# Optimization experiments

Hardware: AMD Instinct MI355X
Metric: run time of the kernel (lower is better)

## Reference

```python
import jax, jax.numpy as jnp
import numpy as np

N = 50000
E = 800000
NFEAT, NHID, NCODE, NCLASS = 512, 256, 64, 40


def setup_inputs() -> dict:
    key = jax.random.key(0)
    ks = jax.random.split(key, 16)
    def glorot(k, shape):
        lim = 1.0 / np.sqrt(shape[0])
        return jax.random.uniform(k, shape, jnp.float32, -lim, lim)
    return {
        "x": jax.random.normal(ks[0], (N, NFEAT), jnp.float32),
        "edge_src": jax.random.randint(ks[1], (E,), 0, N, jnp.int32),
        "edge_dst": jax.random.randint(ks[2], (E,), 0, N, jnp.int32),
        "edge_weight": jax.random.uniform(ks[3], (E,), jnp.float32),
        "eps": jax.random.normal(ks[4], (N, NCODE), jnp.float32),
        # gc1: GraphConvolution(nfeat, nhid)
        "W1": glorot(ks[5], (NFEAT, NHID)),
        "b1": glorot(ks[6], (NHID,)),
        # fc11 / fc12: Linear(nhid, ncode)
        "W_mu": glorot(ks[7], (NHID, NCODE)),
        "b_mu": glorot(ks[8], (NCODE,)),
        "W_lv": glorot(ks[9], (NHID, NCODE)),
        "b_lv": glorot(ks[10], (NCODE,)),
        # fc2: Linear(ncode, nhid)
        "W_dec": glorot(ks[11], (NCODE, NHID)),
        "b_dec": glorot(ks[12], (NHID,)),
        # gc2: GraphConvolution(2*nhid, nclass)
        "W2": glorot(ks[13], (2 * NHID, NCLASS)),
        "b2": glorot(ks[14], (NCLASS,)),
    }


def spmm(edge_src, edge_dst, edge_weight, support):
    # spmm(adj, support): gather rows at src, scale by edge weight, scatter-add to dst
    msgs = support[edge_src] * edge_weight[:, None]  # [E, d]
    return jax.ops.segment_sum(msgs, edge_dst, num_segments=N)


def reference(x, edge_src, edge_dst, edge_weight, eps,
              W1, b1, W_mu, b_mu, W_lv, b_lv, W_dec, b_dec, W2, b2):
    # gc1: relu(spmm(adj, x @ W1) + b1)
    h1 = jax.nn.relu(spmm(edge_src, edge_dst, edge_weight, x @ W1) + b1)
    # dropout is identity in inference mode
    mu = h1 @ W_mu + b_mu
    log_var = h1 @ W_lv + b_lv
    # reparametrize: std = exp(log_var) (as in source, no 0.5 factor)
    z = mu + eps * jnp.exp(log_var)
    # decode
    x1 = jax.nn.relu(z @ W_dec + b_dec)
    x1 = jnp.concatenate([x1, h1], axis=1)  # [N, 2*nhid]
    # gc2
    logits = spmm(edge_src, edge_dst, edge_weight, x1 @ W2) + b2
    return jax.nn.log_softmax(logits, axis=1)
```

## Files before the change

kernel.cpp:

```cpp
#include <hip/hip_runtime.h>
#include <math.h>

#define N_NODES 50000
#define N_EDGES 800000
#define NFEAT 512
#define NHID 256
#define NCODE 64
#define NCLASS 40
#define NCLS_PAD 48
#define NB_SCAN 196

typedef __attribute__((ext_vector_type(8))) short short8;
typedef __attribute__((ext_vector_type(8))) unsigned short ushort8;
typedef __attribute__((ext_vector_type(4))) unsigned short ushort4v;
typedef __attribute__((ext_vector_type(4))) float floatx4;

__device__ inline unsigned short f2bf(float f) {
    unsigned u = __builtin_bit_cast(unsigned, f);
    u += 0x7fff + ((u >> 16) & 1);
    return (unsigned short)(u >> 16);
}
__device__ inline float bf2f(unsigned short h) {
    return __builtin_bit_cast(float, (unsigned)h << 16);
}
__device__ inline unsigned pkbf(float lo, float hi) {
    unsigned r;
    asm("v_cvt_pk_bf16_f32 %0, %1, %2" : "=v"(r) : "v"(lo), "v"(hi));
    return r;
}
__device__ inline void gload_lds16(const void* g, void* l) {
    __builtin_amdgcn_global_load_lds(
        (const __attribute__((address_space(1))) unsigned int*)g,
        (__attribute__((address_space(3))) unsigned int*)l, 16, 0, 0);
}

__global__ __launch_bounds__(256) void hist_kernel(const int* __restrict__ dst,
                                                   int* __restrict__ counts) {
    int t = blockIdx.x * 256 + threadIdx.x;
    if (t < N_EDGES) atomicAdd(&counts[dst[t]], 1);
}

__global__ __launch_bounds__(256) void scan_block_sums(const int* __restrict__ counts,
                                                       int* __restrict__ blockSums) {
    __shared__ int red[256];
    int t = threadIdx.x;
    int i = blockIdx.x * 256 + t;
    red[t] = (i < N_NODES) ? counts[i] : 0;
    __syncthreads();
#pragma unroll
    for (int off = 128; off > 0; off >>= 1) {
        if (t < off) red[t] += red[t + off];
        __syncthreads();
    }
    if (t == 0) blockSums[blockIdx.x] = red[0];
}

__global__ __launch_bounds__(256) void scan_block_offsets(const int* __restrict__ blockSums,
                                                          int* __restrict__ blockOffsets,
                                                          int* __restrict__ offsets) {
    __shared__ int s[256];
    int t = threadIdx.x;
    int v = (t < NB_SCAN) ? blockSums[t] : 0;
    s[t] = v;
    __syncthreads();
#pragma unroll
    for (int off = 1; off < 256; off <<= 1) {
        int x = (t >= off) ? s[t - off] : 0;
        __syncthreads();
        s[t] += x;
        __syncthreads();
    }
    if (t < NB_SCAN) blockOffsets[t] = s[t] - v;
    if (t == 255) offsets[N_NODES] = s[255];
}

__global__ __launch_bounds__(256) void scan_final(const int* __restrict__ counts,
                                                  const int* __restrict__ blockOffsets,
                                                  int* __restrict__ offsets) {
    __shared__ int s[256];
    int t = threadIdx.x;
    int i = blockIdx.x * 256 + t;
    int v = (i < N_NODES) ? counts[i] : 0;
    s[t] = v;
    __syncthreads();
#pragma unroll
    for (int off = 1; off < 256; off <<= 1) {
        int x = (t >= off) ? s[t - off] : 0;
        __syncthreads();
        s[t] += x;
        __syncthreads();
    }
    if (i < N_NODES) offsets[i] = blockOffsets[blockIdx.x] + s[t] - v;
}

__global__ __launch_bounds__(256) void scatter_kernel(const int* __restrict__ dst,
                                                      const int* __restrict__ src,
                                                      const float* __restrict__ w,
                                                      const int* __restrict__ offsets,
                                                      int* __restrict__ cursor,
                                                      int2* __restrict__ edges) {
    int t = blockIdx.x * 256 + threadIdx.x;
    if (t < N_EDGES) {
        int d = dst[t];
        int pos = offsets[d] + atomicAdd(&cursor[d], 1);
        edges[pos] = make_int2(src[t], __builtin_bit_cast(int, w[t]));
    }
}

__global__ __launch_bounds__(256) void wprep_kernel(const float* __restrict__ W1,
                                                    const float* __restrict__ W2,
                                                    const float* __restrict__ W_mu,
                                                    const float* __restrict__ W_lv,
                                                    const float* __restrict__ W_dec,
                                                    unsigned short* __restrict__ W1t,
                                                    unsigned short* __restrict__ W2bt,
                                                    unsigned short* __restrict__ W_mulvt,
                                                    unsigned short* __restrict__ W_dect) {
    int idx = blockIdx.x * 256 + threadIdx.x;
    if (idx < NFEAT * NHID) {
        int k = idx >> 8;
        int n = idx & 255;
        W1t[(size_t)n * NFEAT + k] = f2bf(W1[idx]);
    } else if (idx < NFEAT * NHID + NCLS_PAD * NFEAT) {
        int i2 = idx - NFEAT * NHID;
        int n = i2 >> 9;
        int k = i2 & 511;
        W2bt[i2] = (n < NCLASS) ? f2bf(W2[(size_t)k * NCLASS + n]) : (unsigned short)0;
    } else if (idx < NFEAT * NHID + NCLS_PAD * NFEAT + 128 * 256) {
        int i2 = idx - NFEAT * NHID - NCLS_PAD * NFEAT;
        int j = i2 >> 8;
        int k = i2 & 255;
        float v = (j < 64) ? W_mu[(size_t)k * NCODE + j] : W_lv[(size_t)k * NCODE + (j - 64)];
        W_mulvt[i2] = f2bf(v);
    } else if (idx < NFEAT * NHID + NCLS_PAD * NFEAT + 128 * 256 + 256 * 64) {
        int i2 = idx - NFEAT * NHID - NCLS_PAD * NFEAT - 128 * 256;
        int n = i2 >> 6;
        int k = i2 & 63;
        W_dect[i2] = f2bf(W_dec[(size_t)k * NHID + n]);
    }
}

__global__ __launch_bounds__(256) void gemm1_mfma(const float* __restrict__ A,
                                                  const unsigned short* __restrict__ Bt,
                                                  unsigned short* __restrict__ C) {
    __shared__ unsigned short As[128 * 64];
    __shared__ unsigned short Bs[128 * 64];
    int t = threadIdx.x;
    int wave = t >> 6, lane = t & 63;
    int quad = lane >> 4, m16 = lane & 15;
    int wr = wave >> 1, wc = wave & 1;
    int m0 = blockIdx.x * 128;
    int n0 = blockIdx.y * 128;

    int srow = t >> 3;
    int kcs = (t & 7) ^ (srow & 7);
    const float* Ap[4];
#pragma unroll
    for (int r = 0; r < 4; ++r) {
        int ga = m0 + r * 32 + srow;
        if (ga >= N_NODES) ga = N_NODES - 1;
        Ap[r] = A + (size_t)ga * NFEAT + kcs * 8;
    }
    const unsigned short* Bbase = Bt + (size_t)(n0 + srow) * NFEAT + kcs * 8;

    floatx4 acc[4][4];
#pragma unroll
    for (int m = 0; m < 4; ++m)
#pragma unroll
        for (int n = 0; n < 4; ++n) acc[m][n] = (floatx4){0.f, 0.f, 0.f, 0.f};

    float4 a0[4], a1[4];
#pragma unroll
    for (int r = 0; r < 4; ++r) {
        a0[r] = *(const float4*)(Ap[r]);
        a1[r] = *(const float4*)(Ap[r] + 4);
    }

#pragma unroll
    for (int k0 = 0; k0 < NFEAT; k0 += 64) {
        uint4 aw[4];
#pragma unroll
        for (int r = 0; r < 4; ++r) {
            aw[r].x = pkbf(a0[r].x, a0[r].y);
            aw[r].y = pkbf(a0[r].z, a0[r].w);
            aw[r].z = pkbf(a1[r].x, a1[r].y);
            aw[r].w = pkbf(a1[r].z, a1[r].w);
        }
        __syncthreads();
#pragma unroll
        for (int r = 0; r < 4; ++r)
            gload_lds16(Bbase + (size_t)r * 32 * NFEAT + k0, &Bs[(r * 256 + wave * 64) * 8]);
#pragma unroll
        for (int r = 0; r < 4; ++r) *(uint4*)&As[(r * 256 + t) * 8] = aw[r];
        __syncthreads();
        if (k0 + 64 < NFEAT) {
#pragma unroll
            for (int r = 0; r < 4; ++r) {
                a0[r] = *(const float4*)(Ap[r] + k0 + 64);
                a1[r] = *(const float4*)(Ap[r] + k0 + 68);
            }
        }
#pragma unroll
        for (int c = 0; c < 2; ++c) {
            int sw = ((c * 4 + quad) ^ (m16 & 7)) * 8;
            short8 af[4], bfr[4];
#pragma unroll
            for (int m = 0; m < 4; ++m)
                af[m] = *(const short8*)&As[(wr * 64 + m * 16 + m16) * 64 + sw];
#pragma unroll
            for (int n = 0; n < 4; ++n)
                bfr[n] = *(const short8*)&Bs[(wc * 64 + n * 16 + m16) * 64 + sw];
#pragma unroll
            for (int m = 0; m < 4; ++m)
#pragma unroll
                for (int n = 0; n < 4; ++n)
                    acc[m][n] =
                        __builtin_amdgcn_mfma_f32_16x16x32_bf16(af[m], bfr[n], acc[m][n], 0, 0, 0);
        }
    }
#pragma unroll
    for (int m = 0; m < 4; ++m) {
#pragma unroll
        for (int n = 0; n < 4; ++n) {
            int col = n0 + wc * 64 + n * 16 + m16;
#pragma unroll
            for (int r = 0; r < 4; ++r) {
                int row = m0 + wr * 64 + m * 16 + quad * 4 + r;
                if (row < N_NODES) C[(size_t)row * NHID + col] = f2bf(acc[m][n][r]);
            }
        }
    }
}

__global__ __launch_bounds__(256) void spmm1_kernel(const int* __restrict__ offsets,
                                                    const int2* __restrict__ edges,
                                                    const unsigned short* __restrict__ S1b,
                                                    const float* __restrict__ b1,
                                                    unsigned short* __restrict__ x1cat) {
    int n = blockIdx.x * 4 + (threadIdx.x >> 6);
    int lane = threadIdx.x & 63;
    int beg = offsets[n], end = offsets[n + 1];
    float ax = 0.f, ay = 0.f, az = 0.f, aw = 0.f;
    int i = beg;
    for (; i + 8 <= end; i += 8) {
        int2 e[8];
        ushort4v r[8];
#pragma unroll
        for (int u = 0; u < 8; u++) e[u] = edges[i + u];
#pragma unroll
        for (int u = 0; u < 8; u++)
            r[u] = *(const ushort4v*)&S1b[(size_t)e[u].x * NHID + lane * 4];
#pragma unroll
        for (int u = 0; u < 8; u++) {
            float ww = __builtin_bit_cast(float, e[u].y);
            ax += ww * bf2f(r[u][0]);
            ay += ww * bf2f(r[u][1]);
            az += ww * bf2f(r[u][2]);
            aw += ww * bf2f(r[u][3]);
        }
    }
    for (; i < end; i++) {
        int2 e = edges[i];
        float ww = __builtin_bit_cast(float, e.y);
        ushort4v r = *(const ushort4v*)&S1b[(size_t)e.x * NHID + lane * 4];
        ax += ww * bf2f(r[0]); ay += ww * bf2f(r[1]);
        az += ww * bf2f(r[2]); aw += ww * bf2f(r[3]);
    }
    float4 bb = *(const float4*)&b1[lane * 4];
    ushort4v hb;
    hb[0] = f2bf(fmaxf(ax + bb.x, 0.f));
    hb[1] = f2bf(fmaxf(ay + bb.y, 0.f));
    hb[2] = f2bf(fmaxf(az + bb.z, 0.f));
    hb[3] = f2bf(fmaxf(aw + bb.w, 0.f));
    *(ushort4v*)&x1cat[(size_t)n * (2 * NHID) + NHID + lane * 4] = hb;
}

__global__ __launch_bounds__(256) void mlp_mfma(const unsigned short* __restrict__ x1cat_ro,
                                                const float* __restrict__ eps,
                                                const float* __restrict__ b_mu,
                                                const float* __restrict__ b_lv,
                                                const unsigned short* __restrict__ W_mulvt,
                                                const float* __restrict__ b_dec,
                                                const unsigned short* __restrict__ W_dect,
                                                unsigned short* __restrict__ x1cat) {
    __shared__ float smulv[16][132];
    __shared__ unsigned short z_bf[16][72];
    int t = threadIdx.x;
    int wave = t >> 6, lane = t & 63;
    int quad = lane >> 4, m16 = lane & 15;
    int node0 = blockIdx.x * 16;

    {
        floatx4 acc[2];
        acc[0] = (floatx4){0.f, 0.f, 0.f, 0.f};
        acc[1] = (floatx4){0.f, 0.f, 0.f, 0.f};
        const unsigned short* Abase =
            x1cat_ro + (size_t)(node0 + m16) * 512 + 256 + quad * 8;
        const unsigned short* Bb0 = W_mulvt + (size_t)(wave * 32 + m16) * 256 + quad * 8;
        const unsigned short* Bb1 = Bb0 + 16 * 256;
#pragma unroll
        for (int k0 = 0; k0 < 256; k0 += 32) {
            short8 afrag = *(const short8*)(Abase + k0);
            short8 bf0 = *(const short8*)(Bb0 + k0);
            short8 bf1 = *(const short8*)(Bb1 + k0);
            acc[0] = __builtin_amdgcn_mfma_f32_16x16x32_bf16(afrag, bf0, acc[0], 0, 0, 0);
            acc[1] = __builtin_amdgcn_mfma_f32_16x16x32_bf16(afrag, bf1, acc[1], 0, 0, 0);
        }
#pragma unroll
        for (int nt = 0; nt < 2; nt++) {
            int j = wave * 32 + nt * 16 + m16;
            float bias = (j < 64) ? b_mu[j] : b_lv[j - 64];
#pragma unroll
            for (int r = 0; r < 4; r++)
                smulv[quad * 4 + r][j] = acc[nt][r] + bias;
        }
    }
    __syncthreads();
#pragma unroll
    for (int r = 0; r < 4; r++) {
        int idx = t + r * 256;
        int n = idx >> 6, j = idx & 63;
        float z = smulv[n][j] + eps[(size_t)node0 * NCODE + idx] * expf(smulv[n][64 + j]);
        z_bf[n][j] = f2bf(z);
    }
    __syncthreads();
    {
        floatx4 acc[4];
#pragma unroll
        for (int i = 0; i < 4; i++) acc[i] = (floatx4){0.f, 0.f, 0.f, 0.f};
#pragma unroll
        for (int ks = 0; ks < 2; ks++) {
            int k0 = ks * 32;
            short8 afrag = *(const short8*)&z_bf[m16][k0 + quad * 8];
#pragma unroll
            for (int nt = 0; nt < 4; nt++) {
                int col = wave * 64 + nt * 16 + m16;
                short8 bfrag = *(const short8*)(W_dect + (size_t)col * 64 + k0 + quad * 8);
                acc[nt] = __builtin_amdgcn_mfma_f32_16x16x32_bf16(afrag, bfrag, acc[nt], 0, 0, 0);
            }
        }
#pragma unroll
        for (int nt = 0; nt < 4; nt++) {
            int col = wave * 64 + nt * 16 + m16;
            float bias = b_dec[col];
#pragma unroll
            for (int r = 0; r < 4; r++) {
                int node = node0 + quad * 4 + r;
                x1cat[(size_t)node * 512 + col] = f2bf(fmaxf(acc[nt][r] + bias, 0.f));
            }
        }
    }
}

__global__ __launch_bounds__(256) void gemm2_mfma(const unsigned short* __restrict__ Xb,
                                                  const unsigned short* __restrict__ Bt,
                                                  unsigned short* __restrict__ S2b) {
    __shared__ unsigned short Bs[NCLS_PAD][520];
    int t = threadIdx.x;
    int wave = t >> 6, lane = t & 63;
    int quad = lane >> 4, m16 = lane & 15;
    int m0 = blockIdx.x * 64;

#pragma unroll
    for (int r = 0; r < 12; ++r) {
        int cidx = r * 256 + t;
        int row = cidx >> 6, col = (cidx & 63) * 8;
        *(ushort8*)&Bs[row][col] = *(const ushort8*)&Bt[(size_t)row * NFEAT + col];
    }

    int arow = m0 + wave * 16 + m16;
    if (arow >= N_NODES) arow = N_NODES - 1;
    const unsigned short* Abase = Xb + (size_t)arow * NFEAT + quad * 8;

    floatx4 acc[3];
#pragma unroll
    for (int i = 0; i < 3; i++) acc[i] = (floatx4){0.f, 0.f, 0.f, 0.f};
    __syncthreads();

#pragma unroll
    for (int k0 = 0; k0 < NFEAT; k0 += 32) {
        short8 af = *(const short8*)(Abase + k0);
#pragma unroll
        for (int nt = 0; nt < 3; nt++) {
            short8 bfr = *(const short8*)&Bs[nt * 16 + m16][k0 + quad * 8];
            acc[nt] = __builtin_amdgcn_mfma_f32_16x16x32_bf16(af, bfr, acc[nt], 0, 0, 0);
        }
    }
#pragma unroll
    for (int nt = 0; nt < 3; nt++) {
        int col = nt * 16 + m16;
        if (col < NCLASS) {
#pragma unroll
            for (int r = 0; r < 4; r++) {
                int row = m0 + wave * 16 + quad * 4 + r;
                if (row < N_NODES) S2b[(size_t)row * NCLASS + col] = f2bf(acc[nt][r]);
            }
        }
    }
}

__global__ __launch_bounds__(256) void spmm2_softmax_kernel(const int* __restrict__ offsets,
                                                            const int2* __restrict__ edges,
                                                            const unsigned short* __restrict__ S2b,
                                                            const float* __restrict__ b2,
                                                            float* __restrict__ out) {
    int wave = threadIdx.x >> 6;
    int lane = threadIdx.x & 63;
    int n = blockIdx.x * 4 + wave;
    int beg = offsets[n], end = offsets[n + 1];
    float acc = 0.f;
    int i = beg;
    for (; i + 4 <= end; i += 4) {
        int2 e0 = edges[i], e1 = edges[i + 1], e2 = edges[i + 2], e3 = edges[i + 3];
        float w0 = __builtin_bit_cast(float, e0.y);
        float w1 = __builtin_bit_cast(float, e1.y);
        float w2 = __builtin_bit_cast(float, e2.y);
        float w3 = __builtin_bit_cast(float, e3.y);
        if (lane < NCLASS) {
            float v0 = bf2f(S2b[(size_t)e0.x * NCLASS + lane]);
            float v1 = bf2f(S2b[(size_t)e1.x * NCLASS + lane]);
            float v2 = bf2f(S2b[(size_t)e2.x * NCLASS + lane]);
            float v3 = bf2f(S2b[(size_t)e3.x * NCLASS + lane]);
            acc += w0 * v0 + w1 * v1 + w2 * v2 + w3 * v3;
        }
    }
    for (; i < end; i++) {
        int2 e = edges[i];
        float ww = __builtin_bit_cast(float, e.y);
        if (lane < NCLASS) acc += ww * bf2f(S2b[(size_t)e.x * NCLASS + lane]);
    }
    float v = (lane < NCLASS) ? (acc + b2[lane]) : -INFINITY;
    float m = v;
#pragma unroll
    for (int off = 32; off > 0; off >>= 1) m = fmaxf(m, __shfl_xor(m, off));
    float ex = (lane < NCLASS) ? expf(v - m) : 0.f;
    float ssum = ex;
#pragma unroll
    for (int off = 32; off > 0; off >>= 1) ssum += __shfl_xor(ssum, off);
    if (lane < NCLASS) out[(size_t)n * NCLASS + lane] = v - m - logf(ssum);
}

extern "C" void kernel_launch(void* const* d_in, const int* in_sizes, int n_in,
                              void* d_out, int out_size, void* d_ws, size_t ws_size,
                              hipStream_t stream) {
    const float* x     = (const float*)d_in[0];
    const int*   esrc  = (const int*)d_in[1];
    const int*   edst  = (const int*)d_in[2];
    const float* ew    = (const float*)d_in[3];
    const float* eps   = (const float*)d_in[4];
    const float* W1    = (const float*)d_in[5];
    const float* b1    = (const float*)d_in[6];
    const float* W_mu  = (const float*)d_in[7];
    const float* b_mu  = (const float*)d_in[8];
    const float* W_lv  = (const float*)d_in[9];
    const float* b_lv  = (const float*)d_in[10];
    const float* W_dec = (const float*)d_in[11];
    const float* b_dec = (const float*)d_in[12];
    const float* W2    = (const float*)d_in[13];
    const float* b2    = (const float*)d_in[14];
    float* out = (float*)d_out;

    unsigned short* support1b = (unsigned short*)d_ws;
    unsigned short* x1cat = support1b + (size_t)N_NODES * NHID;
    unsigned short* S2b = x1cat + (size_t)N_NODES * 2 * NHID;
    unsigned short* W1t    = S2b + (size_t)N_NODES * NCLASS;
    unsigned short* W2bt   = W1t + (size_t)NHID * NFEAT;
    unsigned short* W_mulvt = W2bt + (size_t)NCLS_PAD * NFEAT;
    unsigned short* W_dect  = W_mulvt + 128 * 256;
    int*   counts   = (int*)(((size_t)(W_dect + 256 * 64) + 3) & ~(size_t)3);
    int*   cursor   = counts + N_NODES;
    int*   offsets  = cursor + N_NODES;
    int*   blockSums    = offsets + N_NODES + 1;
    int*   blockOffsets = blockSums + NB_SCAN;
    int2*  edges    = (int2*)(blockOffsets + NB_SCAN);
    edges = (int2*)(((size_t)edges + 7) & ~(size_t)7);
    size_t need = (size_t)((char*)(edges + N_EDGES) - (char*)d_ws);
    if (ws_size < need) return;

    hipMemsetAsync(counts, 0, 2 * N_NODES * sizeof(int), stream);
    hist_kernel<<<(N_EDGES + 255) / 256, 256, 0, stream>>>(edst, counts);
    scan_block_sums<<<NB_SCAN, 256, 0, stream>>>(counts, blockSums);
    scan_block_offsets<<<1, 256, 0, stream>>>(blockSums, blockOffsets, offsets);
    scan_final<<<NB_SCAN, 256, 0, stream>>>(counts, blockOffsets, offsets);
    scatter_kernel<<<(N_EDGES + 255) / 256, 256, 0, stream>>>(edst, esrc, ew, offsets, cursor,
                                                              edges);

    wprep_kernel<<<800, 256, 0, stream>>>(W1, W2, W_mu, W_lv, W_dec, W1t, W2bt, W_mulvt, W_dect);
    dim3 g1((N_NODES + 127) / 128, 2);
    gemm1_mfma<<<g1, 256, 0, stream>>>(x, W1t, support1b);
    spmm1_kernel<<<N_NODES / 4, 256, 0, stream>>>(offsets, edges, support1b, b1, x1cat);
    mlp_mfma<<<N_NODES / 16, 256, 0, stream>>>(x1cat, eps, b_mu, b_lv, W_mulvt, b_dec, W_dect,
                                               x1cat);
    gemm2_mfma<<<(N_NODES + 63) / 64, 256, 0, stream>>>(x1cat, W2bt, S2b);
    spmm2_softmax_kernel<<<N_NODES / 4, 256, 0, stream>>>(offsets, edges, S2b, b2, out);
}
```

Baseline: 452.2 us.

## Fuse first SpMM aggregation with the VAE MLP kernel via shared-memory h1 tile

Merges spmm1 and mlp_mfma into one kernel. Each block aggregates 16 nodes, one wave per four nodes, and keeps the relu'd h1 rows in a swizzled LDS tile that feeds the mu/logvar MFMA directly, so the MLP no longer re-reads h1 from global memory and one launch is dropped. h1 is still written to x1cat for gemm2. The cost is less memory-level parallelism per block, since each wave now walks four nodes one after another, and extra LDS use that may lower occupancy.

```diff
diff --git a/kernel.cpp b/kernel.cpp
--- a/kernel.cpp
+++ b/kernel.cpp
@@ -232,77 +232,78 @@
     }
 }
 
-__global__ __launch_bounds__(256) void spmm1_kernel(const int* __restrict__ offsets,
-                                                    const int2* __restrict__ edges,
-                                                    const unsigned short* __restrict__ S1b,
-                                                    const float* __restrict__ b1,
-                                                    unsigned short* __restrict__ x1cat) {
-    int n = blockIdx.x * 4 + (threadIdx.x >> 6);
-    int lane = threadIdx.x & 63;
-    int beg = offsets[n], end = offsets[n + 1];
-    float ax = 0.f, ay = 0.f, az = 0.f, aw = 0.f;
-    int i = beg;
-    for (; i + 8 <= end; i += 8) {
-        int2 e[8];
-        ushort4v r[8];
-#pragma unroll
-        for (int u = 0; u < 8; u++) e[u] = edges[i + u];
-#pragma unroll
-        for (int u = 0; u < 8; u++)
-            r[u] = *(const ushort4v*)&S1b[(size_t)e[u].x * NHID + lane * 4];
-#pragma unroll
-        for (int u = 0; u < 8; u++) {
-            float ww = __builtin_bit_cast(float, e[u].y);
-            ax += ww * bf2f(r[u][0]);
-            ay += ww * bf2f(r[u][1]);
-            az += ww * bf2f(r[u][2]);
-            aw += ww * bf2f(r[u][3]);
-        }
-    }
-    for (; i < end; i++) {
-        int2 e = edges[i];
-        float ww = __builtin_bit_cast(float, e.y);
-        ushort4v r = *(const ushort4v*)&S1b[(size_t)e.x * NHID + lane * 4];
-        ax += ww * bf2f(r[0]); ay += ww * bf2f(r[1]);
-        az += ww * bf2f(r[2]); aw += ww * bf2f(r[3]);
-    }
-    float4 bb = *(const float4*)&b1[lane * 4];
-    ushort4v hb;
-    hb[0] = f2bf(fmaxf(ax + bb.x, 0.f));
-    hb[1] = f2bf(fmaxf(ay + bb.y, 0.f));
-    hb[2] = f2bf(fmaxf(az + bb.z, 0.f));
-    hb[3] = f2bf(fmaxf(aw + bb.w, 0.f));
-    *(ushort4v*)&x1cat[(size_t)n * (2 * NHID) + NHID + lane * 4] = hb;
-}
-
-__global__ __launch_bounds__(256) void mlp_mfma(const unsigned short* __restrict__ x1cat_ro,
-                                                const float* __restrict__ eps,
-                                                const float* __restrict__ b_mu,
-                                                const float* __restrict__ b_lv,
-                                                const unsigned short* __restrict__ W_mulvt,
-                                                const float* __restrict__ b_dec,
-                                                const unsigned short* __restrict__ W_dect,
-                                                unsigned short* __restrict__ x1cat) {
+__global__ __launch_bounds__(256) void spmm1_mlp_kernel(
+    const int* __restrict__ offsets, const int2* __restrict__ edges,
+    const unsigned short* __restrict__ S1b, const float* __restrict__ b1,
+    const float* __restrict__ eps, const float* __restrict__ b_mu,
+    const float* __restrict__ b_lv, const unsigned short* __restrict__ W_mulvt,
+    const float* __restrict__ b_dec, const unsigned short* __restrict__ W_dect,
+    unsigned short* __restrict__ x1cat) {
+    __shared__ unsigned short h1s[16 * 256];
     __shared__ float smulv[16][132];
     __shared__ unsigned short z_bf[16][72];
     int t = threadIdx.x;
     int wave = t >> 6, lane = t & 63;
     int quad = lane >> 4, m16 = lane & 15;
     int node0 = blockIdx.x * 16;
+
+    float4 bb = *(const float4*)&b1[lane * 4];
+#pragma unroll
+    for (int s = 0; s < 4; ++s) {
+        int n = wave * 4 + s;
+        int node = node0 + n;
+        int beg = offsets[node], end = offsets[node + 1];
+        float ax = 0.f, ay = 0.f, az = 0.f, aw = 0.f;
+        int i = beg;
+        for (; i + 8 <= end; i += 8) {
+            int2 e[8];
+            ushort4v r[8];
+#pragma unroll
+            for (int u = 0; u < 8; u++) e[u] = edges[i + u];
+#pragma unroll
+            for (int u = 0; u < 8; u++)
+                r[u] = *(const ushort4v*)&S1b[(size_t)e[u].x * NHID + lane * 4];
+#pragma unroll
+            for (int u = 0; u < 8; u++) {
+                float ww = __builtin_bit_cast(float, e[u].y);
+                ax += ww * bf2f(r[u][0]);
+                ay += ww * bf2f(r[u][1]);
+                az += ww * bf2f(r[u][2]);
+                aw += ww * bf2f(r[u][3]);
+            }
+        }
+        for (; i < end; i++) {
+            int2 e = edges[i];
+            float ww = __builtin_bit_cast(float, e.y);
+            ushort4v r = *(const ushort4v*)&S1b[(size_t)e.x * NHID + lane * 4];
+            ax += ww * bf2f(r[0]);
+            ay += ww * bf2f(r[1]);
+            az += ww * bf2f(r[2]);
+            aw += ww * bf2f(r[3]);
+        }
+        ushort4v hb;
+        hb[0] = f2bf(fmaxf(ax + bb.x, 0.f));
+        hb[1] = f2bf(fmaxf(ay + bb.y, 0.f));
+        hb[2] = f2bf(fmaxf(az + bb.z, 0.f));
+        hb[3] = f2bf(fmaxf(aw + bb.w, 0.f));
+        *(ushort4v*)&x1cat[(size_t)node * (2 * NHID) + NHID + lane * 4] = hb;
+        int chunk = (lane >> 1) ^ (n & 7);
+        *(ushort4v*)&h1s[n * 256 + chunk * 8 + (lane & 1) * 4] = hb;
+    }
+    __syncthreads();
 
     {
         floatx4 acc[2];
         acc[0] = (floatx4){0.f, 0.f, 0.f, 0.f};
         acc[1] = (floatx4){0.f, 0.f, 0.f, 0.f};
-        const unsigned short* Abase =
-            x1cat_ro + (size_t)(node0 + m16) * 512 + 256 + quad * 8;
         const unsigned short* Bb0 = W_mulvt + (size_t)(wave * 32 + m16) * 256 + quad * 8;
         const unsigned short* Bb1 = Bb0 + 16 * 256;
 #pragma unroll
-        for (int k0 = 0; k0 < 256; k0 += 32) {
-            short8 afrag = *(const short8*)(Abase + k0);
-            short8 bf0 = *(const short8*)(Bb0 + k0);
-            short8 bf1 = *(const short8*)(Bb1 + k0);
+        for (int j = 0; j < 8; ++j) {
+            int chunk = (quad + 4 * j) ^ (m16 & 7);
+            short8 afrag = *(const short8*)&h1s[m16 * 256 + chunk * 8];
+            short8 bf0 = *(const short8*)(Bb0 + j * 32);
+            short8 bf1 = *(const short8*)(Bb1 + j * 32);
             acc[0] = __builtin_amdgcn_mfma_f32_16x16x32_bf16(afrag, bf0, acc[0], 0, 0, 0);
             acc[1] = __builtin_amdgcn_mfma_f32_16x16x32_bf16(afrag, bf1, acc[1], 0, 0, 0);
         }
@@ -488,9 +489,8 @@
     wprep_kernel<<<800, 256, 0, stream>>>(W1, W2, W_mu, W_lv, W_dec, W1t, W2bt, W_mulvt, W_dect);
     dim3 g1((N_NODES + 127) / 128, 2);
     gemm1_mfma<<<g1, 256, 0, stream>>>(x, W1t, support1b);
-    spmm1_kernel<<<N_NODES / 4, 256, 0, stream>>>(offsets, edges, support1b, b1, x1cat);
-    mlp_mfma<<<N_NODES / 16, 256, 0, stream>>>(x1cat, eps, b_mu, b_lv, W_mulvt, b_dec, W_dect,
-                                               x1cat);
+    spmm1_mlp_kernel<<<N_NODES / 16, 256, 0, stream>>>(offsets, edges, support1b, b1, eps, b_mu,
+                                                       b_lv, W_mulvt, b_dec, W_dect, x1cat);
     gemm2_mfma<<<(N_NODES + 63) / 64, 256, 0, stream>>>(x1cat, W2bt, S2b);
     spmm2_softmax_kernel<<<N_NODES / 4, 256, 0, stream>>>(offsets, edges, S2b, b2, out);
 }
```

After: 447.6 us. Within noise of the previous version (-1.0%).

## Fuse MLP reparametrization, decoder and gc2 GEMM into one per-wave kernel

Applied to the files above, without the earlier changes.

Merges the mlp kernel and the gc2 GEMM into a single kernel where each wave owns 16 nodes and keeps the decoded x1 in LDS, so the concatenated [N,512] intermediate is never written to or re-read from global memory. spmm1 now writes a compact h1 buffer. W_mu/W_lv are interleaved in the prepped weight so each wave computes matching mu and log_var tiles in registers and applies the reparametrization without a block-level shared buffer or syncs. The cost is higher register use (16 accumulator tiles plus 8 for mu/lv), weights read from global/L2 per wave instead of being staged in LDS, and one kernel launch removed.

```diff
diff --git a/kernel.cpp b/kernel.cpp
--- a/kernel.cpp
+++ b/kernel.cpp
@@ -130,7 +130,9 @@
         int i2 = idx - NFEAT * NHID - NCLS_PAD * NFEAT;
         int j = i2 >> 8;
         int k = i2 & 255;
-        float v = (j < 64) ? W_mu[(size_t)k * NCODE + j] : W_lv[(size_t)k * NCODE + (j - 64)];
+        int q = j >> 5, r5 = j & 31;
+        float v = (r5 < 16) ? W_mu[(size_t)k * NCODE + q * 16 + r5]
+                            : W_lv[(size_t)k * NCODE + q * 16 + (r5 - 16)];
         W_mulvt[i2] = f2bf(v);
     } else if (idx < NFEAT * NHID + NCLS_PAD * NFEAT + 128 * 256 + 256 * 64) {
         int i2 = idx - NFEAT * NHID - NCLS_PAD * NFEAT - 128 * 256;
@@ -236,7 +238,7 @@
                                                     const int2* __restrict__ edges,
                                                     const unsigned short* __restrict__ S1b,
                                                     const float* __restrict__ b1,
-                                                    unsigned short* __restrict__ x1cat) {
+                                                    unsigned short* __restrict__ h1) {
     int n = blockIdx.x * 4 + (threadIdx.x >> 6);
     int lane = threadIdx.x & 63;
     int beg = offsets[n], end = offsets[n + 1];
@@ -272,128 +274,106 @@
     hb[1] = f2bf(fmaxf(ay + bb.y, 0.f));
     hb[2] = f2bf(fmaxf(az + bb.z, 0.f));
     hb[3] = f2bf(fmaxf(aw + bb.w, 0.f));
-    *(ushort4v*)&x1cat[(size_t)n * (2 * NHID) + NHID + lane * 4] = hb;
-}
-
-__global__ __launch_bounds__(256) void mlp_mfma(const unsigned short* __restrict__ x1cat_ro,
-                                                const float* __restrict__ eps,
-                                                const float* __restrict__ b_mu,
-                                                const float* __restrict__ b_lv,
-                                                const unsigned short* __restrict__ W_mulvt,
-                                                const float* __restrict__ b_dec,
-                                                const unsigned short* __restrict__ W_dect,
-                                                unsigned short* __restrict__ x1cat) {
-    __shared__ float smulv[16][132];
-    __shared__ unsigned short z_bf[16][72];
+    *(ushort4v*)&h1[(size_t)n * NHID + lane * 4] = hb;
+}
+
+__global__ __launch_bounds__(256) void mlp_gemm2_kernel(
+    const unsigned short* __restrict__ h1, const float* __restrict__ eps,
+    const float* __restrict__ b_mu, const float* __restrict__ b_lv,
+    const unsigned short* __restrict__ W_mulvt, const float* __restrict__ b_dec,
+    const unsigned short* __restrict__ W_dect, const unsigned short* __restrict__ W2bt,
+    unsigned short* __restrict__ S2b) {
+    __shared__ unsigned short x1s[4][16][264];
+    __shared__ unsigned short zbf[4][16][72];
     int t = threadIdx.x;
     int wave = t >> 6, lane = t & 63;
     int quad = lane >> 4, m16 = lane & 15;
-    int node0 = blockIdx.x * 16;
-
-    {
-        floatx4 acc[2];
-        acc[0] = (floatx4){0.f, 0.f, 0.f, 0.f};
-        acc[1] = (floatx4){0.f, 0.f, 0.f, 0.f};
-        const unsigned short* Abase =
-            x1cat_ro + (size_t)(node0 + m16) * 512 + 256 + quad * 8;
-        const unsigned short* Bb0 = W_mulvt + (size_t)(wave * 32 + m16) * 256 + quad * 8;
-        const unsigned short* Bb1 = Bb0 + 16 * 256;
-#pragma unroll
-        for (int k0 = 0; k0 < 256; k0 += 32) {
-            short8 afrag = *(const short8*)(Abase + k0);
-            short8 bf0 = *(const short8*)(Bb0 + k0);
-            short8 bf1 = *(const short8*)(Bb1 + k0);
-            acc[0] = __builtin_amdgcn_mfma_f32_16x16x32_bf16(afrag, bf0, acc[0], 0, 0, 0);
-            acc[1] = __builtin_amdgcn_mfma_f32_16x16x32_bf16(afrag, bf1, acc[1], 0, 0, 0);
-        }
-#pragma unroll
-        for (int nt = 0; nt < 2; nt++) {
-            int j = wave * 32 + nt * 16 + m16;
-            float bias = (j < 64) ? b_mu[j] : b_lv[j - 64];
-#pragma unroll
-            for (int r = 0; r < 4; r++)
-                smulv[quad * 4 + r][j] = acc[nt][r] + bias;
-        }
-    }
-    __syncthreads();
-#pragma unroll
-    for (int r = 0; r < 4; r++) {
-        int idx = t + r * 256;
-        int n = idx >> 6, j = idx & 63;
-        float z = smulv[n][j] + eps[(size_t)node0 * NCODE + idx] * expf(smulv[n][64 + j]);
-        z_bf[n][j] = f2bf(z);
-    }
-    __syncthreads();
-    {
-        floatx4 acc[4];
-#pragma unroll
-        for (int i = 0; i < 4; i++) acc[i] = (floatx4){0.f, 0.f, 0.f, 0.f};
-#pragma unroll
-        for (int ks = 0; ks < 2; ks++) {
-            int k0 = ks * 32;
-            short8 afrag = *(const short8*)&z_bf[m16][k0 + quad * 8];
-#pragma unroll
-            for (int nt = 0; nt < 4; nt++) {
-                int col = wave * 64 + nt * 16 + m16;
-                short8 bfrag = *(const short8*)(W_dect + (size_t)col * 64 + k0 + quad * 8);
-                acc[nt] = __builtin_amdgcn_mfma_f32_16x16x32_bf16(afrag, bfrag, acc[nt], 0, 0, 0);
-            }
-        }
-#pragma unroll
-        for (int nt = 0; nt < 4; nt++) {
-            int col = wave * 64 + nt * 16 + m16;
-            float bias = b_dec[col];
-#pragma unroll
-            for (int r = 0; r < 4; r++) {
-                int node = node0 + quad * 4 + r;
-                x1cat[(size_t)node * 512 + col] = f2bf(fmaxf(acc[nt][r] + bias, 0.f));
-            }
-        }
-    }
-}
-
-__global__ __launch_bounds__(256) void gemm2_mfma(const unsigned short* __restrict__ Xb,
-                                                  const unsigned short* __restrict__ Bt,
-                                                  unsigned short* __restrict__ S2b) {
-    __shared__ unsigned short Bs[NCLS_PAD][520];
-    int t = threadIdx.x;
-    int wave = t >> 6, lane = t & 63;
-    int quad = lane >> 4, m16 = lane & 15;
-    int m0 = blockIdx.x * 64;
-
-#pragma unroll
-    for (int r = 0; r < 12; ++r) {
-        int cidx = r * 256 + t;
-        int row = cidx >> 6, col = (cidx & 63) * 8;
-        *(ushort8*)&Bs[row][col] = *(const ushort8*)&Bt[(size_t)row * NFEAT + col];
-    }
-
-    int arow = m0 + wave * 16 + m16;
+    int row0 = blockIdx.x * 64 + wave * 16;
+
+    int arow = row0 + m16;
     if (arow >= N_NODES) arow = N_NODES - 1;
-    const unsigned short* Abase = Xb + (size_t)arow * NFEAT + quad * 8;
-
-    floatx4 acc[3];
-#pragma unroll
-    for (int i = 0; i < 3; i++) acc[i] = (floatx4){0.f, 0.f, 0.f, 0.f};
-    __syncthreads();
-
-#pragma unroll
-    for (int k0 = 0; k0 < NFEAT; k0 += 32) {
-        short8 af = *(const short8*)(Abase + k0);
-#pragma unroll
-        for (int nt = 0; nt < 3; nt++) {
-            short8 bfr = *(const short8*)&Bs[nt * 16 + m16][k0 + quad * 8];
-            acc[nt] = __builtin_amdgcn_mfma_f32_16x16x32_bf16(af, bfr, acc[nt], 0, 0, 0);
-        }
-    }
-#pragma unroll
-    for (int nt = 0; nt < 3; nt++) {
+    const unsigned short* Ah = h1 + (size_t)arow * NHID + quad * 8;
+
+    floatx4 amu[4], alv[4];
+#pragma unroll
+    for (int q = 0; q < 4; ++q) {
+        amu[q] = (floatx4){0.f, 0.f, 0.f, 0.f};
+        alv[q] = (floatx4){0.f, 0.f, 0.f, 0.f};
+    }
+#pragma unroll
+    for (int k0 = 0; k0 < NHID; k0 += 32) {
+        short8 af = *(const short8*)(Ah + k0);
+#pragma unroll
+        for (int q = 0; q < 4; ++q) {
+            short8 bm = *(const short8*)(W_mulvt + (size_t)(q * 32 + m16) * 256 + k0 + quad * 8);
+            short8 bl =
+                *(const short8*)(W_mulvt + (size_t)(q * 32 + 16 + m16) * 256 + k0 + quad * 8);
+            amu[q] = __builtin_amdgcn_mfma_f32_16x16x32_bf16(af, bm, amu[q], 0, 0, 0);
+            alv[q] = __builtin_amdgcn_mfma_f32_16x16x32_bf16(af, bl, alv[q], 0, 0, 0);
+        }
+    }
+#pragma unroll
+    for (int q = 0; q < 4; ++q) {
+        int col = q * 16 + m16;
+        float bmu = b_mu[col], blv = b_lv[col];
+#pragma unroll
+        for (int r = 0; r < 4; ++r) {
+            int row = row0 + quad * 4 + r;
+            int er = (row < N_NODES) ? row : N_NODES - 1;
+            float mu = amu[q][r] + bmu;
+            float lv = alv[q][r] + blv;
+            float z = mu + eps[(size_t)er * NCODE + col] * expf(lv);
+            zbf[wave][quad * 4 + r][col] = f2bf(z);
+        }
+    }
+    floatx4 c[16];
+#pragma unroll
+    for (int ct = 0; ct < 16; ++ct) c[ct] = (floatx4){0.f, 0.f, 0.f, 0.f};
+#pragma unroll
+    for (int ks = 0; ks < 2; ++ks) {
+        short8 af = *(const short8*)&zbf[wave][m16][ks * 32 + quad * 8];
+#pragma unroll
+        for (int ct = 0; ct < 16; ++ct) {
+            short8 bfr = *(const short8*)(W_dect + (size_t)(ct * 16 + m16) * 64 + ks * 32 + quad * 8);
+            c[ct] = __builtin_amdgcn_mfma_f32_16x16x32_bf16(af, bfr, c[ct], 0, 0, 0);
+        }
+    }
+#pragma unroll
+    for (int ct = 0; ct < 16; ++ct) {
+        float bias = b_dec[ct * 16 + m16];
+#pragma unroll
+        for (int r = 0; r < 4; ++r)
+            x1s[wave][quad * 4 + r][ct * 16 + m16] = f2bf(fmaxf(c[ct][r] + bias, 0.f));
+    }
+    floatx4 d[3];
+#pragma unroll
+    for (int nt = 0; nt < 3; ++nt) d[nt] = (floatx4){0.f, 0.f, 0.f, 0.f};
+#pragma unroll
+    for (int k0 = 0; k0 < 256; k0 += 32) {
+        short8 af = *(const short8*)&x1s[wave][m16][k0 + quad * 8];
+#pragma unroll
+        for (int nt = 0; nt < 3; ++nt) {
+            short8 bfr = *(const short8*)(W2bt + (size_t)(nt * 16 + m16) * NFEAT + k0 + quad * 8);
+            d[nt] = __builtin_amdgcn_mfma_f32_16x16x32_bf16(af, bfr, d[nt], 0, 0, 0);
+        }
+    }
+#pragma unroll
+    for (int k0 = 256; k0 < 512; k0 += 32) {
+        short8 af = *(const short8*)(Ah + (k0 - 256));
+#pragma unroll
+        for (int nt = 0; nt < 3; ++nt) {
+            short8 bfr = *(const short8*)(W2bt + (size_t)(nt * 16 + m16) * NFEAT + k0 + quad * 8);
+            d[nt] = __builtin_amdgcn_mfma_f32_16x16x32_bf16(af, bfr, d[nt], 0, 0, 0);
+        }
+    }
+#pragma unroll
+    for (int nt = 0; nt < 3; ++nt) {
         int col = nt * 16 + m16;
         if (col < NCLASS) {
 #pragma unroll
-            for (int r = 0; r < 4; r++) {
-                int row = m0 + wave * 16 + quad * 4 + r;
-                if (row < N_NODES) S2b[(size_t)row * NCLASS + col] = f2bf(acc[nt][r]);
+            for (int r = 0; r < 4; ++r) {
+                int row = row0 + quad * 4 + r;
+                if (row < N_NODES) S2b[(size_t)row * NCLASS + col] = f2bf(d[nt][r]);
             }
         }
     }
@@ -461,8 +441,8 @@
     float* out = (float*)d_out;
 
     unsigned short* support1b = (unsigned short*)d_ws;
-    unsigned short* x1cat = support1b + (size_t)N_NODES * NHID;
-    unsigned short* S2b = x1cat + (size_t)N_NODES * 2 * NHID;
+    unsigned short* h1 = support1b + (size_t)N_NODES * NHID;
+    unsigned short* S2b = h1 + (size_t)N_NODES * NHID;
     unsigned short* W1t    = S2b + (size_t)N_NODES * NCLASS;
     unsigned short* W2bt   = W1t + (size_t)NHID * NFEAT;
     unsigned short* W_mulvt = W2bt + (size_t)NCLS_PAD * NFEAT;
@@ -488,9 +468,8 @@
     wprep_kernel<<<800, 256, 0, stream>>>(W1, W2, W_mu, W_lv, W_dec, W1t, W2bt, W_mulvt, W_dect);
     dim3 g1((N_NODES + 127) / 128, 2);
     gemm1_mfma<<<g1, 256, 0, stream>>>(x, W1t, support1b);
-    spmm1_kernel<<<N_NODES / 4, 256, 0, stream>>>(offsets, edges, support1b, b1, x1cat);
-    mlp_mfma<<<N_NODES / 16, 256, 0, stream>>>(x1cat, eps, b_mu, b_lv, W_mulvt, b_dec, W_dect,
-                                               x1cat);
-    gemm2_mfma<<<(N_NODES + 63) / 64, 256, 0, stream>>>(x1cat, W2bt, S2b);
+    spmm1_kernel<<<N_NODES / 4, 256, 0, stream>>>(offsets, edges, support1b, b1, h1);
+    mlp_gemm2_kernel<<<(N_NODES + 63) / 64, 256, 0, stream>>>(h1, eps, b_mu, b_lv, W_mulvt,
+                                                              b_dec, W_dect, W2bt, S2b);
     spmm2_softmax_kernel<<<N_NODES / 4, 256, 0, stream>>>(offsets, edges, S2b, b2, out);
 }
```

Result: slower. 474.6 us (+5.0%).

## Split fused MLP kernel into LDS-tiled mu/logvar GEMM and z-decode GEMM

Applied to the files above, without the earlier changes.

Replaces the fused mlp_mfma kernel, which handled 16 nodes per block and read weights straight from global memory, with two kernels. mulv_mfma tiles 64 nodes per block with the weight slice staged in LDS and writes mu/log_var to a bf16 workspace. zdec_mfma computes z from that buffer and eps in registers, then multiplies by a W_dec held in LDS. The goal is better weight reuse and larger tiles, at the cost of an extra launch, a round trip of the mu/log_var intermediate through global memory, and bf16 rounding of log_var before exp.

```diff
diff --git a/kernel.cpp b/kernel.cpp
--- a/kernel.cpp
+++ b/kernel.cpp
@@ -275,79 +275,112 @@
     *(ushort4v*)&x1cat[(size_t)n * (2 * NHID) + NHID + lane * 4] = hb;
 }
 
-__global__ __launch_bounds__(256) void mlp_mfma(const unsigned short* __restrict__ x1cat_ro,
-                                                const float* __restrict__ eps,
-                                                const float* __restrict__ b_mu,
-                                                const float* __restrict__ b_lv,
-                                                const unsigned short* __restrict__ W_mulvt,
-                                                const float* __restrict__ b_dec,
-                                                const unsigned short* __restrict__ W_dect,
-                                                unsigned short* __restrict__ x1cat) {
-    __shared__ float smulv[16][132];
-    __shared__ unsigned short z_bf[16][72];
+__global__ __launch_bounds__(256) void mulv_mfma(const unsigned short* __restrict__ x1cat,
+                                                 const unsigned short* __restrict__ W_mulvt,
+                                                 const float* __restrict__ b_mu,
+                                                 const float* __restrict__ b_lv,
+                                                 unsigned short* __restrict__ mulv) {
+    __shared__ unsigned short Bs[64][264];
     int t = threadIdx.x;
     int wave = t >> 6, lane = t & 63;
     int quad = lane >> 4, m16 = lane & 15;
-    int node0 = blockIdx.x * 16;
-
-    {
-        floatx4 acc[2];
-        acc[0] = (floatx4){0.f, 0.f, 0.f, 0.f};
-        acc[1] = (floatx4){0.f, 0.f, 0.f, 0.f};
-        const unsigned short* Abase =
-            x1cat_ro + (size_t)(node0 + m16) * 512 + 256 + quad * 8;
-        const unsigned short* Bb0 = W_mulvt + (size_t)(wave * 32 + m16) * 256 + quad * 8;
-        const unsigned short* Bb1 = Bb0 + 16 * 256;
-#pragma unroll
-        for (int k0 = 0; k0 < 256; k0 += 32) {
-            short8 afrag = *(const short8*)(Abase + k0);
-            short8 bf0 = *(const short8*)(Bb0 + k0);
-            short8 bf1 = *(const short8*)(Bb1 + k0);
-            acc[0] = __builtin_amdgcn_mfma_f32_16x16x32_bf16(afrag, bf0, acc[0], 0, 0, 0);
-            acc[1] = __builtin_amdgcn_mfma_f32_16x16x32_bf16(afrag, bf1, acc[1], 0, 0, 0);
-        }
-#pragma unroll
-        for (int nt = 0; nt < 2; nt++) {
-            int j = wave * 32 + nt * 16 + m16;
-            float bias = (j < 64) ? b_mu[j] : b_lv[j - 64];
-#pragma unroll
-            for (int r = 0; r < 4; r++)
-                smulv[quad * 4 + r][j] = acc[nt][r] + bias;
-        }
-    }
+    int m0 = blockIdx.x * 64;
+    int ybase = blockIdx.y * 64;
+
+#pragma unroll
+    for (int r = 0; r < 8; ++r) {
+        int c = r * 256 + t;
+        int row = c >> 5, col = (c & 31) * 8;
+        *(ushort8*)&Bs[row][col] = *(const ushort8*)&W_mulvt[(size_t)(ybase + row) * 256 + col];
+    }
+    int arow = m0 + wave * 16 + m16;
+    if (arow >= N_NODES) arow = N_NODES - 1;
+    const unsigned short* Abase = x1cat + (size_t)arow * 512 + 256 + quad * 8;
+
+    floatx4 acc[4];
+#pragma unroll
+    for (int i = 0; i < 4; ++i) acc[i] = (floatx4){0.f, 0.f, 0.f, 0.f};
     __syncthreads();
-#pragma unroll
-    for (int r = 0; r < 4; r++) {
-        int idx = t + r * 256;
-        int n = idx >> 6, j = idx & 63;
-        float z = smulv[n][j] + eps[(size_t)node0 * NCODE + idx] * expf(smulv[n][64 + j]);
-        z_bf[n][j] = f2bf(z);
-    }
+
+#pragma unroll
+    for (int k0 = 0; k0 < 256; k0 += 32) {
+        short8 af = *(const short8*)(Abase + k0);
+#pragma unroll
+        for (int nt = 0; nt < 4; ++nt) {
+            short8 bfr = *(const short8*)&Bs[nt * 16 + m16][k0 + quad * 8];
+            acc[nt] = __builtin_amdgcn_mfma_f32_16x16x32_bf16(af, bfr, acc[nt], 0, 0, 0);
+        }
+    }
+    const float* bias_v = blockIdx.y ? b_lv : b_mu;
+#pragma unroll
+    for (int nt = 0; nt < 4; ++nt) {
+        int j = nt * 16 + m16;
+        float bias = bias_v[j];
+#pragma unroll
+        for (int r = 0; r < 4; ++r) {
+            int row = m0 + wave * 16 + quad * 4 + r;
+            if (row < N_NODES) mulv[(size_t)row * 128 + ybase + j] = f2bf(acc[nt][r] + bias);
+        }
+    }
+}
+
+__global__ __launch_bounds__(256) void zdec_mfma(const unsigned short* __restrict__ mulv,
+                                                 const float* __restrict__ eps,
+                                                 const unsigned short* __restrict__ W_dect,
+                                                 const float* __restrict__ b_dec,
+                                                 unsigned short* __restrict__ x1cat) {
+    __shared__ unsigned short Bs[256][72];
+    int t = threadIdx.x;
+    int wave = t >> 6, lane = t & 63;
+    int quad = lane >> 4, m16 = lane & 15;
+    int m0 = blockIdx.x * 64;
+
+#pragma unroll
+    for (int r = 0; r < 8; ++r) {
+        int c = r * 256 + t;
+        int row = c >> 3, col = (c & 7) * 8;
+        *(ushort8*)&Bs[row][col] = *(const ushort8*)&W_dect[(size_t)row * 64 + col];
+    }
+    int grow = m0 + wave * 16 + m16;
+    if (grow >= N_NODES) grow = N_NODES - 1;
+
+    floatx4 acc[16];
+#pragma unroll
+    for (int i = 0; i < 16; ++i) acc[i] = (floatx4){0.f, 0.f, 0.f, 0.f};
     __syncthreads();
-    {
-        floatx4 acc[4];
-#pragma unroll
-        for (int i = 0; i < 4; i++) acc[i] = (floatx4){0.f, 0.f, 0.f, 0.f};
-#pragma unroll
-        for (int ks = 0; ks < 2; ks++) {
-            int k0 = ks * 32;
-            short8 afrag = *(const short8*)&z_bf[m16][k0 + quad * 8];
-#pragma unroll
-            for (int nt = 0; nt < 4; nt++) {
-                int col = wave * 64 + nt * 16 + m16;
-                short8 bfrag = *(const short8*)(W_dect + (size_t)col * 64 + k0 + quad * 8);
-                acc[nt] = __builtin_amdgcn_mfma_f32_16x16x32_bf16(afrag, bfrag, acc[nt], 0, 0, 0);
-            }
-        }
-#pragma unroll
-        for (int nt = 0; nt < 4; nt++) {
-            int col = wave * 64 + nt * 16 + m16;
-            float bias = b_dec[col];
-#pragma unroll
-            for (int r = 0; r < 4; r++) {
-                int node = node0 + quad * 4 + r;
-                x1cat[(size_t)node * 512 + col] = f2bf(fmaxf(acc[nt][r] + bias, 0.f));
-            }
+
+#pragma unroll
+    for (int ks = 0; ks < 2; ++ks) {
+        int c0 = ks * 32 + quad * 8;
+        ushort8 mu8 = *(const ushort8*)&mulv[(size_t)grow * 128 + c0];
+        ushort8 lv8 = *(const ushort8*)&mulv[(size_t)grow * 128 + 64 + c0];
+        float4 e0 = *(const float4*)&eps[(size_t)grow * 64 + c0];
+        float4 e1 = *(const float4*)&eps[(size_t)grow * 64 + c0 + 4];
+        ushort8 zz;
+        zz[0] = f2bf(bf2f(mu8[0]) + e0.x * expf(bf2f(lv8[0])));
+        zz[1] = f2bf(bf2f(mu8[1]) + e0.y * expf(bf2f(lv8[1])));
+        zz[2] = f2bf(bf2f(mu8[2]) + e0.z * expf(bf2f(lv8[2])));
+        zz[3] = f2bf(bf2f(mu8[3]) + e0.w * expf(bf2f(lv8[3])));
+        zz[4] = f2bf(bf2f(mu8[4]) + e1.x * expf(bf2f(lv8[4])));
+        zz[5] = f2bf(bf2f(mu8[5]) + e1.y * expf(bf2f(lv8[5])));
+        zz[6] = f2bf(bf2f(mu8[6]) + e1.z * expf(bf2f(lv8[6])));
+        zz[7] = f2bf(bf2f(mu8[7]) + e1.w * expf(bf2f(lv8[7])));
+        short8 af = *(short8*)&zz;
+#pragma unroll
+        for (int nt = 0; nt < 16; ++nt) {
+            short8 bfr = *(const short8*)&Bs[nt * 16 + m16][ks * 32 + quad * 8];
+            acc[nt] = __builtin_amdgcn_mfma_f32_16x16x32_bf16(af, bfr, acc[nt], 0, 0, 0);
+        }
+    }
+#pragma unroll
+    for (int nt = 0; nt < 16; ++nt) {
+        int col = nt * 16 + m16;
+        float bias = b_dec[col];
+#pragma unroll
+        for (int r = 0; r < 4; ++r) {
+            int row = m0 + wave * 16 + quad * 4 + r;
+            if (row < N_NODES)
+                x1cat[(size_t)row * 512 + col] = f2bf(fmaxf(acc[nt][r] + bias, 0.f));
         }
     }
 }
@@ -467,7 +500,8 @@
     unsigned short* W2bt   = W1t + (size_t)NHID * NFEAT;
     unsigned short* W_mulvt = W2bt + (size_t)NCLS_PAD * NFEAT;
     unsigned short* W_dect  = W_mulvt + 128 * 256;
-    int*   counts   = (int*)(((size_t)(W_dect + 256 * 64) + 3) & ~(size_t)3);
+    unsigned short* mulv    = W_dect + 256 * 64;
+    int*   counts   = (int*)(((size_t)(mulv + (size_t)N_NODES * 128) + 3) & ~(size_t)3);
     int*   cursor   = counts + N_NODES;
     int*   offsets  = cursor + N_NODES;
     int*   blockSums    = offsets + N_NODES + 1;
@@ -489,8 +523,9 @@
     dim3 g1((N_NODES + 127) / 128, 2);
     gemm1_mfma<<<g1, 256, 0, stream>>>(x, W1t, support1b);
     spmm1_kernel<<<N_NODES / 4, 256, 0, stream>>>(offsets, edges, support1b, b1, x1cat);
-    mlp_mfma<<<N_NODES / 16, 256, 0, stream>>>(x1cat, eps, b_mu, b_lv, W_mulvt, b_dec, W_dect,
-                                               x1cat);
+    dim3 gm((N_NODES + 63) / 64, 2);
+    mulv_mfma<<<gm, 256, 0, stream>>>(x1cat, W_mulvt, b_mu, b_lv, mulv);
+    zdec_mfma<<<(N_NODES + 63) / 64, 256, 0, stream>>>(mulv, eps, W_dect, b_dec, x1cat);
     gemm2_mfma<<<(N_NODES + 63) / 64, 256, 0, stream>>>(x1cat, W2bt, S2b);
     spmm2_softmax_kernel<<<N_NODES / 4, 256, 0, stream>>>(offsets, edges, S2b, b2, out);
 }
```

Result: faster. 437.5 us (-3.2%).
